# Kernel tuning notes

Measured on AMD Instinct MI355X. Metric: run time of the kernel, lower is better.

The kernel has to match this reference:

```python
import jax, jax.numpy as jnp
import numpy as np


def setup_inputs() -> dict:
    key = jax.random.key(0)
    ks = jax.random.split(key, 4)
    B, H, W, C = 4, 64, 64, 256
    d = C // 8
    x = jax.random.normal(ks[0], (B, H, W, C), dtype=jnp.float32)
    # 1x1 conv weights as [C_in, C_out] matrices (Glorot-ish scale)
    Wq = jax.random.normal(ks[1], (C, d), dtype=jnp.float32) * (1.0 / np.sqrt(C))
    Wk = jax.random.normal(ks[2], (C, d), dtype=jnp.float32) * (1.0 / np.sqrt(C))
    Wv = jax.random.normal(ks[3], (C, C), dtype=jnp.float32) * (1.0 / np.sqrt(C))
    bq = jnp.zeros((d,), dtype=jnp.float32)
    bk = jnp.zeros((d,), dtype=jnp.float32)
    bv = jnp.zeros((C,), dtype=jnp.float32)
    gamma = jnp.float32(0.0)  # matches tf.Variable(0.0)
    return {"x": x, "Wq": Wq, "bq": bq, "Wk": Wk, "bk": bk, "Wv": Wv, "bv": bv, "gamma": gamma}


def reference(x, Wq, bq, Wk, bk, Wv, bv, gamma):
    B, H, W, C = x.shape
    N = H * W
    xf = x.reshape(B, N, C)  # spatial tokens
    q = xf @ Wq + bq  # [B, N, d]
    k = xf @ Wk + bk  # [B, N, d]
    v = xf @ Wv + bv  # [B, N, C]
    energy = jnp.einsum("bnd,bmd->bnm", q, k)  # [B, N, N]
    attn = jax.nn.softmax(energy, axis=-1)
    out = jnp.einsum("bnm,bmc->bnc", attn, v).reshape(B, H, W, C)
    return gamma * out + x
```

## Files before the change

kernel.cpp:

```cpp
#include <hip/hip_runtime.h>
#include <hip/hip_bf16.h>

typedef __attribute__((ext_vector_type(8)))  short short8;
typedef __attribute__((ext_vector_type(4)))  float f32x4;
typedef __attribute__((ext_vector_type(16))) float f32x16;
typedef __attribute__((ext_vector_type(4)))  unsigned int u32x4;

#define LOG2E 1.4426950408889634f

static __device__ __forceinline__ unsigned short f2bf(float f) {
    union { float f; unsigned u; } v; v.f = f;
    unsigned r = v.u + 0x7fffu + ((v.u >> 16) & 1u);
    return (unsigned short)(r >> 16);
}
static __device__ __forceinline__ unsigned cvt_pk_bf16(float lo, float hi) {
    unsigned r;
    asm("v_cvt_pk_bf16_f32 %0, %1, %2" : "=v"(r) : "v"(lo), "v"(hi));
    return r;
}
static __device__ __forceinline__ float exp2_hw(float x) {
    float r;
    asm("v_exp_f32 %0, %1" : "=v"(r) : "v"(x));
    return r;
}

__global__ __launch_bounds__(64) void transpose_w(
    const float* __restrict__ Wq, const float* __restrict__ Wk,
    const float* __restrict__ Wv, unsigned short* __restrict__ Wtf)
{
    const int g  = blockIdx.x;
    const int ct = g >> 3, kk = g & 7;
    const int l  = threadIdx.x;
    const int col = ct * 16 + (l & 15);
    const int k0  = kk * 32 + (l >> 4) * 8;
    const float* W; int c, ldw;
    if (col < 32)      { W = Wq; c = col;      ldw = 32;  }
    else if (col < 64) { W = Wk; c = col - 32; ldw = 32;  }
    else               { W = Wv; c = col - 64; ldw = 256; }
    ushort4 o0, o1;
    o0.x = f2bf(W[(size_t)(k0 + 0) * ldw + c]);
    o0.y = f2bf(W[(size_t)(k0 + 1) * ldw + c]);
    o0.z = f2bf(W[(size_t)(k0 + 2) * ldw + c]);
    o0.w = f2bf(W[(size_t)(k0 + 3) * ldw + c]);
    o1.x = f2bf(W[(size_t)(k0 + 4) * ldw + c]);
    o1.y = f2bf(W[(size_t)(k0 + 5) * ldw + c]);
    o1.z = f2bf(W[(size_t)(k0 + 6) * ldw + c]);
    o1.w = f2bf(W[(size_t)(k0 + 7) * ldw + c]);
    *reinterpret_cast<ushort4*>(Wtf + (size_t)g * 512 + l * 8)     = o0;
    *reinterpret_cast<ushort4*>(Wtf + (size_t)g * 512 + l * 8 + 4) = o1;
}

__global__ __launch_bounds__(256) void proj_kernel(
    const float* __restrict__ x, const unsigned short* __restrict__ Wtf,
    const float* __restrict__ bq, const float* __restrict__ bk,
    const float* __restrict__ bv,
    unsigned short* __restrict__ Qb, unsigned short* __restrict__ Kf,
    unsigned short* __restrict__ Vf)
{
    __shared__ unsigned short x_lds[64][264];
    const int tid = threadIdx.x;
    const int M0  = (blockIdx.x >> 1) * 64;
    const int ctb = (blockIdx.x & 1) * 10;

    #pragma unroll
    for (int j = 0; j < 16; ++j) {
        int idx = j * 256 + tid;
        int row = idx >> 6;
        int qc  = idx & 63;
        const float4 v = *reinterpret_cast<const float4*>(x + (size_t)(M0 + row) * 256 + qc * 4);
        ushort4 o;
        o.x = f2bf(v.x); o.y = f2bf(v.y); o.z = f2bf(v.z); o.w = f2bf(v.w);
        *reinterpret_cast<ushort4*>(&x_lds[row][qc * 4]) = o;
    }
    __syncthreads();

    const int w  = tid >> 6;
    const int l  = tid & 63;
    const int lr = l & 15;
    const int lg = l >> 4;

    short8 a[8];
    #pragma unroll
    for (int kk = 0; kk < 8; ++kk)
        a[kk] = *reinterpret_cast<const short8*>(&x_lds[w * 16 + lr][kk * 32 + lg * 8]);

    const int b   = M0 >> 12;
    const int kt  = (M0 & 4095) >> 6;

    for (int ct = ctb; ct < ctb + 10; ++ct) {
        const int col = ct * 16 + lr;
        f32x4 acc = {0.f, 0.f, 0.f, 0.f};
        #pragma unroll
        for (int kk = 0; kk < 8; ++kk) {
            const short8 bfr = *reinterpret_cast<const short8*>(
                Wtf + ((size_t)ct * 8 + kk) * 512 + l * 8);
            acc = __builtin_amdgcn_mfma_f32_16x16x32_bf16(a[kk], bfr, acc, 0, 0, 0);
        }
        const int rbase = M0 + w * 16 + lg * 4;
        if (ct < 2) {
            const float bias = bq[col];
            #pragma unroll
            for (int r = 0; r < 4; ++r)
                Qb[(size_t)(rbase + r) * 32 + col] = f2bf((acc[r] + bias) * LOG2E);
        } else if (ct < 4) {
            const int colp = col - 32;
            const float bias = bk[colp];
            const int dd = colp >> 4, hj = (colp >> 3) & 1, jj = colp & 7;
            #pragma unroll
            for (int r = 0; r < 4; ++r) {
                const int tt = (rbase + r) & 4095;
                const size_t e = (size_t)b * 131072 + (size_t)kt * 2048
                               + (((tt >> 5) & 1) * 2 + dd) * 512
                               + (hj * 32 + (tt & 31)) * 8 + jj;
                Kf[e] = f2bf(acc[r] + bias);
            }
        } else {
            const int colp = col - 64;
            const float bias = bv[colp];
            const int kk_f = w;
            const int hi_v = (lg >> 1) & 1;
            const int j0   = (lg & 1) * 4;
            const size_t e = (size_t)b * 1048576 + (size_t)kt * 16384
                           + (colp >> 5) * 2048 + kk_f * 512
                           + (hi_v * 32 + (colp & 31)) * 8 + j0;
            ushort4 o;
            o.x = f2bf(acc[0] + bias); o.y = f2bf(acc[1] + bias);
            o.z = f2bf(acc[2] + bias); o.w = f2bf(acc[3] + bias);
            *reinterpret_cast<ushort4*>(Vf + e) = o;
        }
    }
}

__global__ __launch_bounds__(128, 2) void attn_kernel(
    const unsigned short* __restrict__ Qb, const unsigned short* __restrict__ Kf,
    const unsigned short* __restrict__ Vf, const float* __restrict__ x,
    const float* __restrict__ gamma_p, float* __restrict__ out)
{
    __shared__ float O_sh[4][16][64];
    __shared__ float l_sh[2][32];

    const int i  = blockIdx.x;
    const int b  = (i & 7) >> 1;
    const int t  = ((i >> 3) << 1) | (i & 1);
    const int qt = t >> 1;
    const int cg = t & 1;

    const int tid = threadIdx.x;
    const int kh  = tid >> 6;
    const int l   = tid & 63;
    const int l5  = l & 31;
    const int hi  = l >> 5;

    const size_t bN = (size_t)b * 4096;
    const int q0 = qt * 32;
    const int c0 = cg * 128;

    const unsigned short* Kfb = Kf + (size_t)b * 131072 + l * 8;
    const unsigned short* Vfb = Vf + (size_t)b * 1048576 + (c0 >> 5) * 2048 + l * 8;

    short8 qb[2];
    #pragma unroll
    for (int dd = 0; dd < 2; ++dd)
        qb[dd] = *reinterpret_cast<const short8*>(
            Qb + (bN + (size_t)(q0 + l5)) * 32 + dd * 16 + hi * 8);

    short8 onesB;
    #pragma unroll
    for (int j = 0; j < 8; ++j) onesB[j] = (short)0x3F80;

    f32x16 Oa[4];
    #pragma unroll
    for (int ct = 0; ct < 4; ++ct)
        #pragma unroll
        for (int r = 0; r < 16; ++r) Oa[ct][r] = 0.f;
    f32x16 Os;
    #pragma unroll
    for (int r = 0; r < 16; ++r) Os[r] = 0.f;

    f32x16 z;
    #pragma unroll
    for (int r = 0; r < 16; ++r) z[r] = 0.f;

    const int kt0 = kh * 32;

    auto loadK = [&](short8 (&kA)[2][2], int ktg) {
        const unsigned short* kp = Kfb + (size_t)ktg * 2048;
        #pragma unroll
        for (int ks = 0; ks < 2; ++ks)
            #pragma unroll
            for (int dd = 0; dd < 2; ++dd)
                kA[ks][dd] = *reinterpret_cast<const short8*>(kp + (ks * 2 + dd) * 512);
    };

    short8 pa[4];
    auto build_pa = [&](const f32x16& p, int base) {
        unsigned c[8];
        #pragma unroll
        for (int n = 0; n < 8; ++n)
            c[n] = cvt_pk_bf16(exp2_hw(p[2 * n]), exp2_hw(p[2 * n + 1]));
        #pragma unroll
        for (int k2 = 0; k2 < 2; ++k2) {
            unsigned d0 = c[4 * k2 + 0], d2 = c[4 * k2 + 2];
            unsigned d1 = c[4 * k2 + 1], d3 = c[4 * k2 + 3];
            asm("v_permlane32_swap_b32 %0, %1" : "+v"(d0), "+v"(d2));
            asm("v_permlane32_swap_b32 %0, %1" : "+v"(d1), "+v"(d3));
            u32x4 u = {d0, d1, d2, d3};
            pa[base + k2] = __builtin_bit_cast(short8, u);
        }
    };

    auto body = [&](short8 (&kcur)[2][2], short8 (&knxt)[2][2], int ktg, int ktgn) {
        const unsigned short* vp = Vfb + (size_t)ktg * 16384;
        short8 vf[4][4];
        #pragma unroll
        for (int ct = 0; ct < 4; ++ct)
            #pragma unroll
            for (int kk = 0; kk < 4; ++kk)
                vf[ct][kk] = *reinterpret_cast<const short8*>(vp + ct * 2048 + kk * 512);
        loadK(knxt, ktgn);
        {
            f32x16 p = __builtin_amdgcn_mfma_f32_32x32x16_bf16(kcur[0][0], qb[0], z, 0, 0, 0);
            p        = __builtin_amdgcn_mfma_f32_32x32x16_bf16(kcur[0][1], qb[1], p, 0, 0, 0);
            build_pa(p, 0);
        }
        {
            f32x16 p = __builtin_amdgcn_mfma_f32_32x32x16_bf16(kcur[1][0], qb[0], z, 0, 0, 0);
            p        = __builtin_amdgcn_mfma_f32_32x32x16_bf16(kcur[1][1], qb[1], p, 0, 0, 0);
            build_pa(p, 2);
        }
        #pragma unroll
        for (int kk = 0; kk < 4; ++kk)
            Os = __builtin_amdgcn_mfma_f32_32x32x16_bf16(pa[kk], onesB, Os, 0, 0, 0);
        __builtin_amdgcn_s_setprio(1);
        #pragma unroll
        for (int ct = 0; ct < 4; ++ct)
            #pragma unroll
            for (int kk = 0; kk < 4; ++kk)
                Oa[ct] = __builtin_amdgcn_mfma_f32_32x32x16_bf16(pa[kk], vf[ct][kk], Oa[ct], 0, 0, 0);
        __builtin_amdgcn_s_setprio(0);
    };

    short8 kA0[2][2], kA1[2][2];
    loadK(kA0, kt0);
    for (int kt = 0; kt < 32; kt += 2) {
        body(kA0, kA1, kt0 + kt, kt0 + kt + 1);
        body(kA1, kA0, kt0 + kt + 1, kt0 + ((kt + 2) & 31));
    }

    if (l5 == 0) {
        #pragma unroll
        for (int r = 0; r < 16; ++r)
            l_sh[kh][(r & 3) + 8 * (r >> 2) + 4 * hi] = Os[r];
    }
    #pragma unroll
    for (int ct = 0; ct < 4; ++ct)
        if ((ct >> 1) != kh) {
            #pragma unroll
            for (int r = 0; r < 16; ++r)
                O_sh[ct][r][hi * 32 + l5] = Oa[ct][r];
        }
    __syncthreads();

    const float gamma = gamma_p[0];
    #pragma unroll
    for (int ct = 0; ct < 4; ++ct)
        if ((ct >> 1) == kh) {
            #pragma unroll
            for (int r = 0; r < 16; ++r) {
                const int qr = (r & 3) + 8 * (r >> 2) + 4 * hi;
                const float ltot = l_sh[0][qr] + l_sh[1][qr];
                const float osum = Oa[ct][r] + O_sh[ct][r][hi * 32 + l5];
                const size_t idx = (bN + (size_t)(q0 + qr)) * 256 + c0 + ct * 32 + l5;
                out[idx] = gamma * (osum / ltot) + x[idx];
            }
        }
}

extern "C" void kernel_launch(void* const* d_in, const int* in_sizes, int n_in,
                              void* d_out, int out_size, void* d_ws, size_t ws_size,
                              hipStream_t stream) {
    const float* x     = (const float*)d_in[0];
    const float* Wq    = (const float*)d_in[1];
    const float* bq    = (const float*)d_in[2];
    const float* Wk    = (const float*)d_in[3];
    const float* bk    = (const float*)d_in[4];
    const float* Wv    = (const float*)d_in[5];
    const float* bv    = (const float*)d_in[6];
    const float* gamma = (const float*)d_in[7];
    float* out = (float*)d_out;

    unsigned short* Qb  = (unsigned short*)d_ws;
    unsigned short* Kf  = Qb + (size_t)16384 * 32;
    unsigned short* Vf  = Kf + (size_t)16384 * 32;
    unsigned short* Wtf = Vf + (size_t)4 * 256 * 4096;

    transpose_w<<<160, 64, 0, stream>>>(Wq, Wk, Wv, Wtf);
    proj_kernel<<<512, 256, 0, stream>>>(x, Wtf, bq, bk, bv, Qb, Kf, Vf);
    attn_kernel<<<1024, 128, 0, stream>>>(Qb, Kf, Vf, x, gamma, out);
}
```

Baseline: 88.47 us.

## Retile attention blocks to 64 queries by 64 channels and sum rows on VALU

Each block now handles 64 query rows and 64 output channels instead of 32 queries and 128 channels, so every loaded V fragment feeds two query halves and total V traffic halves. The price is that Q·K^T and exp2 are recomputed by four channel groups per query tile instead of two, which doubles that work. The ones-vector MFMA that produced softmax row sums is replaced by VALU accumulation of the exponentials plus a cross-half shuffle, and the shared-memory reduction is reshaped to match.

```diff
diff --git a/kernel.cpp b/kernel.cpp
--- a/kernel.cpp
+++ b/kernel.cpp
@@ -136,14 +136,14 @@
     const unsigned short* __restrict__ Vf, const float* __restrict__ x,
     const float* __restrict__ gamma_p, float* __restrict__ out)
 {
-    __shared__ float O_sh[4][16][64];
-    __shared__ float l_sh[2][32];
+    __shared__ float O_sh[2][2][16][64];
+    __shared__ float l_sh[2][2][32];
 
     const int i  = blockIdx.x;
     const int b  = (i & 7) >> 1;
     const int t  = ((i >> 3) << 1) | (i & 1);
-    const int qt = t >> 1;
-    const int cg = t & 1;
+    const int qt = t >> 2;
+    const int cg = t & 3;
 
     const int tid = threadIdx.x;
     const int kh  = tid >> 6;
@@ -152,30 +152,28 @@
     const int hi  = l >> 5;
 
     const size_t bN = (size_t)b * 4096;
-    const int q0 = qt * 32;
-    const int c0 = cg * 128;
+    const int q0 = qt * 64;
+    const int c0 = cg * 64;
 
     const unsigned short* Kfb = Kf + (size_t)b * 131072 + l * 8;
-    const unsigned short* Vfb = Vf + (size_t)b * 1048576 + (c0 >> 5) * 2048 + l * 8;
-
-    short8 qb[2];
-    #pragma unroll
-    for (int dd = 0; dd < 2; ++dd)
-        qb[dd] = *reinterpret_cast<const short8*>(
-            Qb + (bN + (size_t)(q0 + l5)) * 32 + dd * 16 + hi * 8);
-
-    short8 onesB;
-    #pragma unroll
-    for (int j = 0; j < 8; ++j) onesB[j] = (short)0x3F80;
-
-    f32x16 Oa[4];
-    #pragma unroll
-    for (int ct = 0; ct < 4; ++ct)
-        #pragma unroll
-        for (int r = 0; r < 16; ++r) Oa[ct][r] = 0.f;
-    f32x16 Os;
-    #pragma unroll
-    for (int r = 0; r < 16; ++r) Os[r] = 0.f;
+    const unsigned short* Vfb = Vf + (size_t)b * 1048576 + (size_t)cg * 4096 + l * 8;
+
+    short8 qb[2][2];
+    #pragma unroll
+    for (int qh = 0; qh < 2; ++qh)
+        #pragma unroll
+        for (int dd = 0; dd < 2; ++dd)
+            qb[qh][dd] = *reinterpret_cast<const short8*>(
+                Qb + (bN + (size_t)(q0 + qh * 32 + l5)) * 32 + dd * 16 + hi * 8);
+
+    f32x16 Oa[2][2];
+    #pragma unroll
+    for (int qh = 0; qh < 2; ++qh)
+        #pragma unroll
+        for (int ct = 0; ct < 2; ++ct)
+            #pragma unroll
+            for (int r = 0; r < 16; ++r) Oa[qh][ct][r] = 0.f;
+    float lsA[2] = {0.f, 0.f}, lsB[2] = {0.f, 0.f};
 
     f32x16 z;
     #pragma unroll
@@ -192,12 +190,16 @@
                 kA[ks][dd] = *reinterpret_cast<const short8*>(kp + (ks * 2 + dd) * 512);
     };
 
-    short8 pa[4];
-    auto build_pa = [&](const f32x16& p, int base) {
+    short8 pa[2][4];
+    auto build_pa = [&](int qh, const f32x16& p, int base) {
         unsigned c[8];
         #pragma unroll
-        for (int n = 0; n < 8; ++n)
-            c[n] = cvt_pk_bf16(exp2_hw(p[2 * n]), exp2_hw(p[2 * n + 1]));
+        for (int n = 0; n < 8; ++n) {
+            const float e0 = exp2_hw(p[2 * n]);
+            const float e1 = exp2_hw(p[2 * n + 1]);
+            lsA[qh] += e0; lsB[qh] += e1;
+            c[n] = cvt_pk_bf16(e0, e1);
+        }
         #pragma unroll
         for (int k2 = 0; k2 < 2; ++k2) {
             unsigned d0 = c[4 * k2 + 0], d2 = c[4 * k2 + 2];
@@ -205,38 +207,36 @@
             asm("v_permlane32_swap_b32 %0, %1" : "+v"(d0), "+v"(d2));
             asm("v_permlane32_swap_b32 %0, %1" : "+v"(d1), "+v"(d3));
             u32x4 u = {d0, d1, d2, d3};
-            pa[base + k2] = __builtin_bit_cast(short8, u);
+            pa[qh][base + k2] = __builtin_bit_cast(short8, u);
         }
     };
 
     auto body = [&](short8 (&kcur)[2][2], short8 (&knxt)[2][2], int ktg, int ktgn) {
         const unsigned short* vp = Vfb + (size_t)ktg * 16384;
-        short8 vf[4][4];
-        #pragma unroll
-        for (int ct = 0; ct < 4; ++ct)
+        short8 vf[2][4];
+        #pragma unroll
+        for (int ct = 0; ct < 2; ++ct)
             #pragma unroll
             for (int kk = 0; kk < 4; ++kk)
                 vf[ct][kk] = *reinterpret_cast<const short8*>(vp + ct * 2048 + kk * 512);
         loadK(knxt, ktgn);
-        {
-            f32x16 p = __builtin_amdgcn_mfma_f32_32x32x16_bf16(kcur[0][0], qb[0], z, 0, 0, 0);
-            p        = __builtin_amdgcn_mfma_f32_32x32x16_bf16(kcur[0][1], qb[1], p, 0, 0, 0);
-            build_pa(p, 0);
-        }
-        {
-            f32x16 p = __builtin_amdgcn_mfma_f32_32x32x16_bf16(kcur[1][0], qb[0], z, 0, 0, 0);
-            p        = __builtin_amdgcn_mfma_f32_32x32x16_bf16(kcur[1][1], qb[1], p, 0, 0, 0);
-            build_pa(p, 2);
-        }
-        #pragma unroll
-        for (int kk = 0; kk < 4; ++kk)
-            Os = __builtin_amdgcn_mfma_f32_32x32x16_bf16(pa[kk], onesB, Os, 0, 0, 0);
+        #pragma unroll
+        for (int qh = 0; qh < 2; ++qh)
+            #pragma unroll
+            for (int ks = 0; ks < 2; ++ks) {
+                f32x16 p = __builtin_amdgcn_mfma_f32_32x32x16_bf16(kcur[ks][0], qb[qh][0], z, 0, 0, 0);
+                p        = __builtin_amdgcn_mfma_f32_32x32x16_bf16(kcur[ks][1], qb[qh][1], p, 0, 0, 0);
+                build_pa(qh, p, ks * 2);
+            }
         __builtin_amdgcn_s_setprio(1);
         #pragma unroll
-        for (int ct = 0; ct < 4; ++ct)
-            #pragma unroll
-            for (int kk = 0; kk < 4; ++kk)
-                Oa[ct] = __builtin_amdgcn_mfma_f32_32x32x16_bf16(pa[kk], vf[ct][kk], Oa[ct], 0, 0, 0);
+        for (int ct = 0; ct < 2; ++ct)
+            #pragma unroll
+            for (int qh = 0; qh < 2; ++qh)
+                #pragma unroll
+                for (int kk = 0; kk < 4; ++kk)
+                    Oa[qh][ct] = __builtin_amdgcn_mfma_f32_32x32x16_bf16(
+                        pa[qh][kk], vf[ct][kk], Oa[qh][ct], 0, 0, 0);
         __builtin_amdgcn_s_setprio(0);
     };
 
@@ -247,33 +247,37 @@
         body(kA1, kA0, kt0 + kt + 1, kt0 + ((kt + 2) & 31));
     }
 
-    if (l5 == 0) {
-        #pragma unroll
-        for (int r = 0; r < 16; ++r)
-            l_sh[kh][(r & 3) + 8 * (r >> 2) + 4 * hi] = Os[r];
-    }
-    #pragma unroll
-    for (int ct = 0; ct < 4; ++ct)
-        if ((ct >> 1) != kh) {
-            #pragma unroll
-            for (int r = 0; r < 16; ++r)
-                O_sh[ct][r][hi * 32 + l5] = Oa[ct][r];
+    #pragma unroll
+    for (int qh = 0; qh < 2; ++qh) {
+        float s = lsA[qh] + lsB[qh];
+        s += __shfl_xor(s, 32);
+        if (hi == 0) l_sh[kh][qh][l5] = s;
+    }
+    #pragma unroll
+    for (int qh = 0; qh < 2; ++qh)
+        if (qh != kh) {
+            #pragma unroll
+            for (int ct = 0; ct < 2; ++ct)
+                #pragma unroll
+                for (int r = 0; r < 16; ++r)
+                    O_sh[qh][ct][r][hi * 32 + l5] = Oa[qh][ct][r];
         }
     __syncthreads();
 
     const float gamma = gamma_p[0];
-    #pragma unroll
-    for (int ct = 0; ct < 4; ++ct)
-        if ((ct >> 1) == kh) {
+    {
+        const int qh = kh;
+        #pragma unroll
+        for (int ct = 0; ct < 2; ++ct)
             #pragma unroll
             for (int r = 0; r < 16; ++r) {
                 const int qr = (r & 3) + 8 * (r >> 2) + 4 * hi;
-                const float ltot = l_sh[0][qr] + l_sh[1][qr];
-                const float osum = Oa[ct][r] + O_sh[ct][r][hi * 32 + l5];
-                const size_t idx = (bN + (size_t)(q0 + qr)) * 256 + c0 + ct * 32 + l5;
+                const float ltot = l_sh[0][qh][qr] + l_sh[1][qh][qr];
+                const float osum = Oa[qh][ct][r] + O_sh[qh][ct][r][hi * 32 + l5];
+                const size_t idx = (bN + (size_t)(q0 + qh * 32 + qr)) * 256 + c0 + ct * 32 + l5;
                 out[idx] = gamma * (osum / ltot) + x[idx];
             }
-        }
+    }
 }
 
 extern "C" void kernel_launch(void* const* d_in, const int* in_sizes, int n_in,
```

Measured after the change: 167.5 us. 1.89x slower.

## Stage V tiles in double-buffered LDS shared across 64-query blocks

Applied to the files above, without the earlier changes.

The attention kernel moves from 1024 blocks of two waves, each splitting keys and covering a 32-query by 128-channel tile, to 256 blocks of four waves covering 64 queries and all 256 channels. Each key tile of V is loaded cooperatively into a double-buffered LDS area, so V global traffic is shared by both query halves. The cross-wave split-K reduction through shared memory is removed, and the row sum is accumulated in VALU instead of an extra MFMA against a ones matrix. The costs are a block barrier per key tile, a grid of only 256 blocks at one block per CU, and added LDS traffic.

```diff
diff --git a/kernel.cpp b/kernel.cpp
--- a/kernel.cpp
+++ b/kernel.cpp
@@ -131,73 +131,83 @@
     }
 }
 
-__global__ __launch_bounds__(128, 2) void attn_kernel(
+__global__ __launch_bounds__(256, 1) void attn_kernel(
     const unsigned short* __restrict__ Qb, const unsigned short* __restrict__ Kf,
     const unsigned short* __restrict__ Vf, const float* __restrict__ x,
     const float* __restrict__ gamma_p, float* __restrict__ out)
 {
-    __shared__ float O_sh[4][16][64];
+    __shared__ unsigned short Vlds[2][16384];
     __shared__ float l_sh[2][32];
 
     const int i  = blockIdx.x;
-    const int b  = (i & 7) >> 1;
-    const int t  = ((i >> 3) << 1) | (i & 1);
-    const int qt = t >> 1;
-    const int cg = t & 1;
+    const int b  = i & 3;
+    const int qt = i >> 2;
 
     const int tid = threadIdx.x;
-    const int kh  = tid >> 6;
+    const int w   = tid >> 6;
+    const int qh  = w >> 1;
+    const int cs  = w & 1;
     const int l   = tid & 63;
     const int l5  = l & 31;
     const int hi  = l >> 5;
 
     const size_t bN = (size_t)b * 4096;
-    const int q0 = qt * 32;
-    const int c0 = cg * 128;
+    const int q0 = qt * 64;
 
     const unsigned short* Kfb = Kf + (size_t)b * 131072 + l * 8;
-    const unsigned short* Vfb = Vf + (size_t)b * 1048576 + (c0 >> 5) * 2048 + l * 8;
+    const unsigned short* Vst = Vf + (size_t)b * 1048576 + (size_t)w * 4096 + l * 8;
 
     short8 qb[2];
     #pragma unroll
     for (int dd = 0; dd < 2; ++dd)
         qb[dd] = *reinterpret_cast<const short8*>(
-            Qb + (bN + (size_t)(q0 + l5)) * 32 + dd * 16 + hi * 8);
-
-    short8 onesB;
-    #pragma unroll
-    for (int j = 0; j < 8; ++j) onesB[j] = (short)0x3F80;
+            Qb + (bN + (size_t)(q0 + qh * 32 + l5)) * 32 + dd * 16 + hi * 8);
 
     f32x16 Oa[4];
     #pragma unroll
     for (int ct = 0; ct < 4; ++ct)
         #pragma unroll
         for (int r = 0; r < 16; ++r) Oa[ct][r] = 0.f;
-    f32x16 Os;
-    #pragma unroll
-    for (int r = 0; r < 16; ++r) Os[r] = 0.f;
+    float lsA = 0.f, lsB = 0.f;
 
     f32x16 z;
     #pragma unroll
     for (int r = 0; r < 16; ++r) z[r] = 0.f;
 
-    const int kt0 = kh * 32;
-
-    auto loadK = [&](short8 (&kA)[2][2], int ktg) {
-        const unsigned short* kp = Kfb + (size_t)ktg * 2048;
+    short8 kA[2][2];
+    auto loadK = [&](int kt) {
+        const unsigned short* kp = Kfb + (size_t)kt * 2048;
         #pragma unroll
         for (int ks = 0; ks < 2; ++ks)
             #pragma unroll
             for (int dd = 0; dd < 2; ++dd)
                 kA[ks][dd] = *reinterpret_cast<const short8*>(kp + (ks * 2 + dd) * 512);
+    };
+
+    short8 st[8];
+    auto stageIssue = [&](int kt) {
+        const unsigned short* vp = Vst + (size_t)kt * 16384;
+        #pragma unroll
+        for (int s = 0; s < 8; ++s)
+            st[s] = *reinterpret_cast<const short8*>(vp + s * 512);
+    };
+    auto stageWrite = [&](int buf) {
+        unsigned short* dst = &Vlds[buf][w * 4096 + l * 8];
+        #pragma unroll
+        for (int s = 0; s < 8; ++s)
+            *reinterpret_cast<short8*>(dst + s * 512) = st[s];
     };
 
     short8 pa[4];
     auto build_pa = [&](const f32x16& p, int base) {
         unsigned c[8];
         #pragma unroll
-        for (int n = 0; n < 8; ++n)
-            c[n] = cvt_pk_bf16(exp2_hw(p[2 * n]), exp2_hw(p[2 * n + 1]));
+        for (int n = 0; n < 8; ++n) {
+            const float e0 = exp2_hw(p[2 * n]);
+            const float e1 = exp2_hw(p[2 * n + 1]);
+            lsA += e0; lsB += e1;
+            c[n] = cvt_pk_bf16(e0, e1);
+        }
         #pragma unroll
         for (int k2 = 0; k2 < 2; ++k2) {
             unsigned d0 = c[4 * k2 + 0], d2 = c[4 * k2 + 2];
@@ -209,70 +219,54 @@
         }
     };
 
-    auto body = [&](short8 (&kcur)[2][2], short8 (&knxt)[2][2], int ktg, int ktgn) {
-        const unsigned short* vp = Vfb + (size_t)ktg * 16384;
-        short8 vf[4][4];
-        #pragma unroll
-        for (int ct = 0; ct < 4; ++ct)
+    stageIssue(0);
+    loadK(0);
+    stageWrite(0);
+    __syncthreads();
+
+    int cur = 0;
+    for (int kt = 0; kt < 64; ++kt) {
+        stageIssue((kt + 1) & 63);
+        f32x16 p0 = __builtin_amdgcn_mfma_f32_32x32x16_bf16(kA[0][0], qb[0], z, 0, 0, 0);
+        p0        = __builtin_amdgcn_mfma_f32_32x32x16_bf16(kA[0][1], qb[1], p0, 0, 0, 0);
+        f32x16 p1 = __builtin_amdgcn_mfma_f32_32x32x16_bf16(kA[1][0], qb[0], z, 0, 0, 0);
+        p1        = __builtin_amdgcn_mfma_f32_32x32x16_bf16(kA[1][1], qb[1], p1, 0, 0, 0);
+        loadK((kt + 1) & 63);
+        build_pa(p0, 0);
+        build_pa(p1, 2);
+        const unsigned short* vl = &Vlds[cur][cs * 8192 + l * 8];
+        __builtin_amdgcn_s_setprio(1);
+        #pragma unroll
+        for (int ct = 0; ct < 4; ++ct) {
+            short8 vfr[4];
             #pragma unroll
             for (int kk = 0; kk < 4; ++kk)
-                vf[ct][kk] = *reinterpret_cast<const short8*>(vp + ct * 2048 + kk * 512);
-        loadK(knxt, ktgn);
-        {
-            f32x16 p = __builtin_amdgcn_mfma_f32_32x32x16_bf16(kcur[0][0], qb[0], z, 0, 0, 0);
-            p        = __builtin_amdgcn_mfma_f32_32x32x16_bf16(kcur[0][1], qb[1], p, 0, 0, 0);
-            build_pa(p, 0);
-        }
-        {
-            f32x16 p = __builtin_amdgcn_mfma_f32_32x32x16_bf16(kcur[1][0], qb[0], z, 0, 0, 0);
-            p        = __builtin_amdgcn_mfma_f32_32x32x16_bf16(kcur[1][1], qb[1], p, 0, 0, 0);
-            build_pa(p, 2);
-        }
-        #pragma unroll
-        for (int kk = 0; kk < 4; ++kk)
-            Os = __builtin_amdgcn_mfma_f32_32x32x16_bf16(pa[kk], onesB, Os, 0, 0, 0);
-        __builtin_amdgcn_s_setprio(1);
-        #pragma unroll
-        for (int ct = 0; ct < 4; ++ct)
+                vfr[kk] = *reinterpret_cast<const short8*>(vl + ct * 2048 + kk * 512);
             #pragma unroll
             for (int kk = 0; kk < 4; ++kk)
-                Oa[ct] = __builtin_amdgcn_mfma_f32_32x32x16_bf16(pa[kk], vf[ct][kk], Oa[ct], 0, 0, 0);
+                Oa[ct] = __builtin_amdgcn_mfma_f32_32x32x16_bf16(pa[kk], vfr[kk], Oa[ct], 0, 0, 0);
+        }
         __builtin_amdgcn_s_setprio(0);
-    };
-
-    short8 kA0[2][2], kA1[2][2];
-    loadK(kA0, kt0);
-    for (int kt = 0; kt < 32; kt += 2) {
-        body(kA0, kA1, kt0 + kt, kt0 + kt + 1);
-        body(kA1, kA0, kt0 + kt + 1, kt0 + ((kt + 2) & 31));
+        stageWrite(cur ^ 1);
+        __syncthreads();
+        cur ^= 1;
     }
 
-    if (l5 == 0) {
-        #pragma unroll
-        for (int r = 0; r < 16; ++r)
-            l_sh[kh][(r & 3) + 8 * (r >> 2) + 4 * hi] = Os[r];
-    }
+    float lsum = lsA + lsB;
+    lsum += __shfl_xor(lsum, 32);
+    if (hi == 0) l_sh[qh][l5] = lsum;
+    __syncthreads();
+
+    const float gamma = gamma_p[0];
     #pragma unroll
     for (int ct = 0; ct < 4; ++ct)
-        if ((ct >> 1) != kh) {
-            #pragma unroll
-            for (int r = 0; r < 16; ++r)
-                O_sh[ct][r][hi * 32 + l5] = Oa[ct][r];
-        }
-    __syncthreads();
-
-    const float gamma = gamma_p[0];
-    #pragma unroll
-    for (int ct = 0; ct < 4; ++ct)
-        if ((ct >> 1) == kh) {
-            #pragma unroll
-            for (int r = 0; r < 16; ++r) {
-                const int qr = (r & 3) + 8 * (r >> 2) + 4 * hi;
-                const float ltot = l_sh[0][qr] + l_sh[1][qr];
-                const float osum = Oa[ct][r] + O_sh[ct][r][hi * 32 + l5];
-                const size_t idx = (bN + (size_t)(q0 + qr)) * 256 + c0 + ct * 32 + l5;
-                out[idx] = gamma * (osum / ltot) + x[idx];
-            }
+        #pragma unroll
+        for (int r = 0; r < 16; ++r) {
+            const int qr = (r & 3) + 8 * (r >> 2) + 4 * hi;
+            const float ltot = l_sh[qh][qr];
+            const size_t idx = (bN + (size_t)(q0 + qh * 32 + qr)) * 256
+                             + cs * 128 + ct * 32 + l5;
+            out[idx] = gamma * (Oa[ct][r] / ltot) + x[idx];
         }
 }
 
@@ -296,5 +290,5 @@
 
     transpose_w<<<160, 64, 0, stream>>>(Wq, Wk, Wv, Wtf);
     proj_kernel<<<512, 256, 0, stream>>>(x, Wtf, bq, bk, bv, Qb, Kf, Vf);
-    attn_kernel<<<1024, 128, 0, stream>>>(Qb, Kf, Vf, x, gamma, out);
-}
+    attn_kernel<<<256, 256, 0, stream>>>(Qb, Kf, Vf, x, gamma, out);
+}
```

New measurement: 109.3 us. 23.6% more time.

## Split attention key range across four waves and compute row sums with VALU

Applied to the files above, without the earlier changes.

The attention kernel now uses 256 threads, four waves per block, each handling a quarter of the key range. Partial outputs are reduced through a larger shared buffer. The row-sum MFMA against a ones matrix is replaced by VALU accumulation of the exponentials plus a cross-half shuffle. V fragments are loaded per column tile just before use instead of all up front, and K is single-buffered. This cuts per-wave serial work and register pressure, at the cost of more shared memory (about 48KB) and a heavier reduction epilogue.

```diff
diff --git a/kernel.cpp b/kernel.cpp
--- a/kernel.cpp
+++ b/kernel.cpp
@@ -131,13 +131,13 @@
     }
 }
 
-__global__ __launch_bounds__(128, 2) void attn_kernel(
+__global__ __launch_bounds__(256, 3) void attn_kernel(
     const unsigned short* __restrict__ Qb, const unsigned short* __restrict__ Kf,
     const unsigned short* __restrict__ Vf, const float* __restrict__ x,
     const float* __restrict__ gamma_p, float* __restrict__ out)
 {
-    __shared__ float O_sh[4][16][64];
-    __shared__ float l_sh[2][32];
+    __shared__ float O_sh[4][3][16][64];
+    __shared__ float l_sh[4][32];
 
     const int i  = blockIdx.x;
     const int b  = (i & 7) >> 1;
@@ -146,7 +146,7 @@
     const int cg = t & 1;
 
     const int tid = threadIdx.x;
-    const int kh  = tid >> 6;
+    const int w   = tid >> 6;
     const int l   = tid & 63;
     const int l5  = l & 31;
     const int hi  = l >> 5;
@@ -164,26 +164,17 @@
         qb[dd] = *reinterpret_cast<const short8*>(
             Qb + (bN + (size_t)(q0 + l5)) * 32 + dd * 16 + hi * 8);
 
-    short8 onesB;
-    #pragma unroll
-    for (int j = 0; j < 8; ++j) onesB[j] = (short)0x3F80;
-
     f32x16 Oa[4];
     #pragma unroll
     for (int ct = 0; ct < 4; ++ct)
         #pragma unroll
         for (int r = 0; r < 16; ++r) Oa[ct][r] = 0.f;
-    f32x16 Os;
-    #pragma unroll
-    for (int r = 0; r < 16; ++r) Os[r] = 0.f;
-
-    f32x16 z;
-    #pragma unroll
-    for (int r = 0; r < 16; ++r) z[r] = 0.f;
-
-    const int kt0 = kh * 32;
-
-    auto loadK = [&](short8 (&kA)[2][2], int ktg) {
+    float lsA = 0.f, lsB = 0.f;
+
+    const int kt0 = w * 16;
+
+    short8 kA[2][2];
+    auto loadK = [&](int ktg) {
         const unsigned short* kp = Kfb + (size_t)ktg * 2048;
         #pragma unroll
         for (int ks = 0; ks < 2; ++ks)
@@ -194,14 +185,18 @@
 
     short8 pa[4];
     auto build_pa = [&](const f32x16& p, int base) {
-        unsigned c[8];
-        #pragma unroll
-        for (int n = 0; n < 8; ++n)
-            c[n] = cvt_pk_bf16(exp2_hw(p[2 * n]), exp2_hw(p[2 * n + 1]));
         #pragma unroll
         for (int k2 = 0; k2 < 2; ++k2) {
-            unsigned d0 = c[4 * k2 + 0], d2 = c[4 * k2 + 2];
-            unsigned d1 = c[4 * k2 + 1], d3 = c[4 * k2 + 3];
+            unsigned c[4];
+            #pragma unroll
+            for (int n = 0; n < 4; ++n) {
+                const int m = k2 * 8 + 2 * n;
+                const float e0 = exp2_hw(p[m]);
+                const float e1 = exp2_hw(p[m + 1]);
+                lsA += e0; lsB += e1;
+                c[n] = cvt_pk_bf16(e0, e1);
+            }
+            unsigned d0 = c[0], d2 = c[2], d1 = c[1], d3 = c[3];
             asm("v_permlane32_swap_b32 %0, %1" : "+v"(d0), "+v"(d2));
             asm("v_permlane32_swap_b32 %0, %1" : "+v"(d1), "+v"(d3));
             u32x4 u = {d0, d1, d2, d3};
@@ -209,71 +204,68 @@
         }
     };
 
-    auto body = [&](short8 (&kcur)[2][2], short8 (&knxt)[2][2], int ktg, int ktgn) {
+    auto body = [&](int ktg, int ktgn) {
         const unsigned short* vp = Vfb + (size_t)ktg * 16384;
-        short8 vf[4][4];
-        #pragma unroll
-        for (int ct = 0; ct < 4; ++ct)
+        f32x16 z;
+        #pragma unroll
+        for (int r = 0; r < 16; ++r) z[r] = 0.f;
+        {
+            f32x16 p = __builtin_amdgcn_mfma_f32_32x32x16_bf16(kA[0][0], qb[0], z, 0, 0, 0);
+            p        = __builtin_amdgcn_mfma_f32_32x32x16_bf16(kA[0][1], qb[1], p, 0, 0, 0);
+            build_pa(p, 0);
+        }
+        {
+            f32x16 p = __builtin_amdgcn_mfma_f32_32x32x16_bf16(kA[1][0], qb[0], z, 0, 0, 0);
+            p        = __builtin_amdgcn_mfma_f32_32x32x16_bf16(kA[1][1], qb[1], p, 0, 0, 0);
+            loadK(ktgn);
+            build_pa(p, 2);
+        }
+        __builtin_amdgcn_s_setprio(1);
+        #pragma unroll
+        for (int ct = 0; ct < 4; ++ct) {
+            short8 vfr[4];
             #pragma unroll
             for (int kk = 0; kk < 4; ++kk)
-                vf[ct][kk] = *reinterpret_cast<const short8*>(vp + ct * 2048 + kk * 512);
-        loadK(knxt, ktgn);
-        {
-            f32x16 p = __builtin_amdgcn_mfma_f32_32x32x16_bf16(kcur[0][0], qb[0], z, 0, 0, 0);
-            p        = __builtin_amdgcn_mfma_f32_32x32x16_bf16(kcur[0][1], qb[1], p, 0, 0, 0);
-            build_pa(p, 0);
-        }
-        {
-            f32x16 p = __builtin_amdgcn_mfma_f32_32x32x16_bf16(kcur[1][0], qb[0], z, 0, 0, 0);
-            p        = __builtin_amdgcn_mfma_f32_32x32x16_bf16(kcur[1][1], qb[1], p, 0, 0, 0);
-            build_pa(p, 2);
-        }
-        #pragma unroll
-        for (int kk = 0; kk < 4; ++kk)
-            Os = __builtin_amdgcn_mfma_f32_32x32x16_bf16(pa[kk], onesB, Os, 0, 0, 0);
-        __builtin_amdgcn_s_setprio(1);
-        #pragma unroll
-        for (int ct = 0; ct < 4; ++ct)
+                vfr[kk] = *reinterpret_cast<const short8*>(vp + ct * 2048 + kk * 512);
             #pragma unroll
             for (int kk = 0; kk < 4; ++kk)
-                Oa[ct] = __builtin_amdgcn_mfma_f32_32x32x16_bf16(pa[kk], vf[ct][kk], Oa[ct], 0, 0, 0);
+                Oa[ct] = __builtin_amdgcn_mfma_f32_32x32x16_bf16(pa[kk], vfr[kk], Oa[ct], 0, 0, 0);
+        }
         __builtin_amdgcn_s_setprio(0);
     };
 
-    short8 kA0[2][2], kA1[2][2];
-    loadK(kA0, kt0);
-    for (int kt = 0; kt < 32; kt += 2) {
-        body(kA0, kA1, kt0 + kt, kt0 + kt + 1);
-        body(kA1, kA0, kt0 + kt + 1, kt0 + ((kt + 2) & 31));
-    }
-
-    if (l5 == 0) {
-        #pragma unroll
-        for (int r = 0; r < 16; ++r)
-            l_sh[kh][(r & 3) + 8 * (r >> 2) + 4 * hi] = Os[r];
+    loadK(kt0);
+    for (int kt = 0; kt < 16; ++kt)
+        body(kt0 + kt, kt0 + ((kt + 1) & 15));
+
+    {
+        float s = lsA + lsB;
+        s += __shfl_xor(s, 32);
+        if (hi == 0) l_sh[w][l5] = s;
     }
     #pragma unroll
     for (int ct = 0; ct < 4; ++ct)
-        if ((ct >> 1) != kh) {
+        if (ct != w) {
+            const int slot = ct - (ct > w ? 1 : 0);
             #pragma unroll
             for (int r = 0; r < 16; ++r)
-                O_sh[ct][r][hi * 32 + l5] = Oa[ct][r];
+                O_sh[w][slot][r][hi * 32 + l5] = Oa[ct][r];
         }
     __syncthreads();
 
     const float gamma = gamma_p[0];
     #pragma unroll
-    for (int ct = 0; ct < 4; ++ct)
-        if ((ct >> 1) == kh) {
-            #pragma unroll
-            for (int r = 0; r < 16; ++r) {
-                const int qr = (r & 3) + 8 * (r >> 2) + 4 * hi;
-                const float ltot = l_sh[0][qr] + l_sh[1][qr];
-                const float osum = Oa[ct][r] + O_sh[ct][r][hi * 32 + l5];
-                const size_t idx = (bN + (size_t)(q0 + qr)) * 256 + c0 + ct * 32 + l5;
-                out[idx] = gamma * (osum / ltot) + x[idx];
-            }
-        }
+    for (int r = 0; r < 16; ++r) {
+        const int qr = (r & 3) + 8 * (r >> 2) + 4 * hi;
+        const float ltot = l_sh[0][qr] + l_sh[1][qr] + l_sh[2][qr] + l_sh[3][qr];
+        float osum = Oa[w][r];
+        #pragma unroll
+        for (int p = 0; p < 4; ++p)
+            if (p != w)
+                osum += O_sh[p][w - (w > p ? 1 : 0)][r][hi * 32 + l5];
+        const size_t idx = (bN + (size_t)(q0 + qr)) * 256 + c0 + w * 32 + l5;
+        out[idx] = gamma * (osum / ltot) + x[idx];
+    }
 }
 
 extern "C" void kernel_launch(void* const* d_in, const int* in_sizes, int n_in,
@@ -296,5 +288,5 @@
 
     transpose_w<<<160, 64, 0, stream>>>(Wq, Wk, Wv, Wtf);
     proj_kernel<<<512, 256, 0, stream>>>(x, Wtf, bq, bk, bv, Qb, Kf, Vf);
-    attn_kernel<<<1024, 128, 0, stream>>>(Qb, Kf, Vf, x, gamma, out);
-}
+    attn_kernel<<<1024, 256, 0, stream>>>(Qb, Kf, Vf, x, gamma, out);
+}
```

New measurement: 140.5 us. 58.8% more time.
